# Kernel optimization log

Hardware: AMD Instinct MI355X
Metric: run time of the kernel (lower is better)

Reference implementation:

```python
import jax, jax.numpy as jnp
import numpy as np

N_TOKENS = 65536   # number of embeddings to quantize
CODE_DIM = 768     # embedding dim
NUM_CODES = 4096   # codebook size


def setup_inputs() -> dict:
    key = jax.random.key(0)
    k1, k2 = jax.random.split(key)
    x = jax.random.normal(k1, (N_TOKENS, CODE_DIM), dtype=jnp.float32)
    codebook = jax.random.normal(k2, (NUM_CODES, CODE_DIM), dtype=jnp.float32)
    return {"x": x, "codebook": codebook}


def reference(x, codebook):
    # argmin over squared distances == argmin over cdist (sqrt is monotone).
    x2 = jnp.sum(x * x, axis=-1, keepdims=True)          # [N, 1]
    c2 = jnp.sum(codebook * codebook, axis=-1)           # [K]
    dist = x2 + c2[None, :] - 2.0 * jnp.einsum('nd,kd->nk', x, codebook)  # [N, K]
    indices = jnp.argmin(dist, axis=-1)                  # [N] int
    quantized = codebook[indices]                        # gather [N, D]
    # straight-through estimator: forward = quantized, grad flows to x
    q_ste = x + jax.lax.stop_gradient(quantized - x)
    return q_ste, indices
```

## Files before the change

kernel.cpp:

```cpp
#include <hip/hip_runtime.h>

#define N_TOKENS  65536
#define CODE_DIM  768
#define NUM_CODES 4096

#define MARGIN 0.006f
#define FLTMAX 3.4028235e38f

typedef __attribute__((ext_vector_type(8))) short bf16x8;
typedef __attribute__((ext_vector_type(4))) float f32x4;

__device__ __forceinline__ unsigned short f2bf(float f) {
  unsigned int u = __float_as_uint(f);
  unsigned int r = (u + 0x7fffu + ((u >> 16) & 1u)) >> 16;
  return (unsigned short)r;
}
__device__ __forceinline__ float bf2f(unsigned short h) {
  return __uint_as_float(((unsigned int)h) << 16);
}
__device__ __forceinline__ void gl2lds16(const void* g, void* l) {
  __builtin_amdgcn_global_load_lds(
      (const __attribute__((address_space(1))) unsigned int*)g,
      (__attribute__((address_space(3))) unsigned int*)l, 16, 0, 0);
}

__global__ __launch_bounds__(256) void vq_convert_kernel(
    const float* __restrict__ x, const float* __restrict__ cb,
    unsigned short* __restrict__ xh, unsigned short* __restrict__ xl,
    unsigned short* __restrict__ cbh, unsigned short* __restrict__ cbl,
    float* __restrict__ x2, float* __restrict__ c2, int* __restrict__ fcnt) {
  if (blockIdx.x == 0 && threadIdx.x == 0) *fcnt = 0;
  const int wave = threadIdx.x >> 6;
  const int lane = threadIdx.x & 63;
  const int row  = blockIdx.x * 4 + wave;
  const float* src;
  unsigned short *hdst, *ldst;
  float* ndst;
  if (row < N_TOKENS) {
    src = x + (size_t)row * CODE_DIM;
    hdst = xh + (size_t)row * CODE_DIM;
    ldst = xl + (size_t)row * CODE_DIM;
    ndst = x2 + row;
  } else {
    const int r = row - N_TOKENS;
    if (r >= NUM_CODES) return;
    src = cb + (size_t)r * CODE_DIM;
    hdst = cbh + (size_t)r * CODE_DIM;
    ldst = cbl + (size_t)r * CODE_DIM;
    ndst = c2 + r;
  }
  const float4* s4 = (const float4*)src;
  ushort4* h4 = (ushort4*)hdst;
  ushort4* l4 = (ushort4*)ldst;
  float acc = 0.f;
#pragma unroll
  for (int i = 0; i < 3; ++i) {
    float4 f = s4[lane + 64 * i];
    ushort4 h, l;
    h.x = f2bf(f.x); l.x = f2bf(f.x - bf2f(h.x));
    h.y = f2bf(f.y); l.y = f2bf(f.y - bf2f(h.y));
    h.z = f2bf(f.z); l.z = f2bf(f.z - bf2f(h.z));
    h.w = f2bf(f.w); l.w = f2bf(f.w - bf2f(h.w));
    h4[lane + 64 * i] = h;
    l4[lane + 64 * i] = l;
    acc += (f.x * f.x + f.y * f.y) + (f.z * f.z + f.w * f.w);
  }
#pragma unroll
  for (int off = 32; off > 0; off >>= 1) acc += __shfl_down(acc, off, 64);
  if (lane == 0) *ndst = acc;
}

#define BT 256

__global__ __launch_bounds__(512, 2) void vq_mfma_kernel(
    const unsigned short* __restrict__ xh, const unsigned short* __restrict__ xl,
    const unsigned short* __restrict__ cbh, const unsigned short* __restrict__ cbl,
    const float* __restrict__ c2, int* __restrict__ out_idx,
    int* __restrict__ fcnt, int* __restrict__ flist) {
  __shared__ __align__(16) unsigned short sA[3][BT * 64];
  __shared__ __align__(16) unsigned short sB[3][128 * 64];
  __shared__ float redv[512], redsv[512];
  __shared__ int   redi[512];

  const int tid = threadIdx.x;
  const int wave = tid >> 6, lane = tid & 63;
  const int l15 = lane & 15, quad = lane >> 4;
  const int wr = wave >> 1, wc = wave & 1;
  const int tokBase = blockIdx.x * BT;

  const int lr = lane >> 3;
  const int cc = (lane & 7) ^ lr;
  const int hsel = cc >> 2;
  const int coff = (cc & 3) * 8;
  const unsigned short* pAsrc = hsel ? xl : xh;
  const unsigned short* pBsrc = hsel ? cbl : cbh;
  const size_t aOff = (size_t)(tokBase + wave * 32 + lr) * CODE_DIM + coff;
  const size_t bOff = (size_t)(wave * 16 + lr) * CODE_DIM + coff;

  const int aposh = (quad ^ (l15 & 7)) * 8;
  const int aBaseH = (wr * 64 + l15) * 64 + aposh;
  const int aBaseL = (wr * 64 + l15) * 64 + (aposh ^ 32);
  const int bBaseH = (wc * 64 + l15) * 64 + aposh;
  const int bBaseL = (wc * 64 + l15) * 64 + (aposh ^ 32);

  float v[4][4], sv[4][4];
  int bi[4][4];
#pragma unroll
  for (int i = 0; i < 4; ++i)
#pragma unroll
    for (int r = 0; r < 4; ++r) { v[i][r] = FLTMAX; sv[i][r] = FLTMAX; bi[i][r] = 0; }

  auto STAGE = [&](int slot, int sk0, size_t bbase) {
#pragma unroll
    for (int t = 0; t < 4; ++t)
      gl2lds16(pAsrc + aOff + (size_t)t * (8 * CODE_DIM) + sk0,
               &sA[slot][(wave * 32 + t * 8) * 64]);
#pragma unroll
    for (int t = 0; t < 2; ++t)
      gl2lds16(pBsrc + bbase + bOff + (size_t)t * (8 * CODE_DIM) + sk0,
               &sB[slot][(wave * 16 + t * 8) * 64]);
  };

  STAGE(0, 0, 0);
  STAGE(1, 32, 0);
  asm volatile("s_waitcnt vmcnt(6)" ::: "memory");
  __builtin_amdgcn_s_barrier();
  __builtin_amdgcn_sched_barrier(0);

  int skt = 0, sks = 2;
  for (int kt = 0; kt < NUM_CODES / 128; ++kt) {
    f32x4 acc[4][4];
#pragma unroll
    for (int i = 0; i < 4; ++i)
#pragma unroll
      for (int j = 0; j < 4; ++j) acc[i][j] = (f32x4){0.f, 0.f, 0.f, 0.f};

    for (int ksq = 0; ksq < CODE_DIM / 32; ++ksq) {
      const int slot = ksq % 3;
      const bool more = !(kt == NUM_CODES / 128 - 1 && ksq >= 22);
      if (more) {
        STAGE((ksq + 2) % 3, sks * 32, (size_t)skt * (128 * CODE_DIM));
        if (++sks == CODE_DIM / 32) { sks = 0; ++skt; }
      }

      const unsigned short* As = sA[slot];
      const unsigned short* Bs = sB[slot];
      bf16x8 fah[4], fal[4], fbh[4], fbl[4];
#pragma unroll
      for (int i = 0; i < 4; ++i) {
        fah[i] = *(const bf16x8*)(As + aBaseH + i * 1024);
        fal[i] = *(const bf16x8*)(As + aBaseL + i * 1024);
      }
#pragma unroll
      for (int j = 0; j < 4; ++j) {
        fbh[j] = *(const bf16x8*)(Bs + bBaseH + j * 1024);
        fbl[j] = *(const bf16x8*)(Bs + bBaseL + j * 1024);
      }
      __builtin_amdgcn_s_setprio(1);
#pragma unroll
      for (int i = 0; i < 4; ++i)
#pragma unroll
        for (int j = 0; j < 4; ++j) {
          acc[i][j] = __builtin_amdgcn_mfma_f32_16x16x32_bf16(fah[i], fbh[j], acc[i][j], 0, 0, 0);
          acc[i][j] = __builtin_amdgcn_mfma_f32_16x16x32_bf16(fah[i], fbl[j], acc[i][j], 0, 0, 0);
          acc[i][j] = __builtin_amdgcn_mfma_f32_16x16x32_bf16(fal[i], fbh[j], acc[i][j], 0, 0, 0);
        }
      __builtin_amdgcn_s_setprio(0);
      if (more) asm volatile("s_waitcnt vmcnt(6)" ::: "memory");
      else      asm volatile("s_waitcnt vmcnt(0)" ::: "memory");
      __builtin_amdgcn_s_barrier();
      __builtin_amdgcn_sched_barrier(0);
    }

    const int kbase = kt * 128;
#pragma unroll
    for (int j = 0; j < 4; ++j) {
      const int kcol = kbase + wc * 64 + j * 16 + l15;
      const float c2j = c2[kcol];
#pragma unroll
      for (int i = 0; i < 4; ++i)
#pragma unroll
        for (int r = 0; r < 4; ++r) {
          float s = fmaf(-2.0f, acc[i][j][r], c2j);
          float vo = v[i][r];
          sv[i][r] = fminf(sv[i][r], fmaxf(s, vo));
          bool lt = s < vo;
          v[i][r]  = lt ? s : vo;
          bi[i][r] = lt ? kcol : bi[i][r];
        }
    }
  }

#pragma unroll
  for (int i = 0; i < 4; ++i)
#pragma unroll
    for (int r = 0; r < 4; ++r) {
      float vv = v[i][r], svv = sv[i][r];
      int ii = bi[i][r];
#pragma unroll
      for (int m = 1; m < 16; m <<= 1) {
        float ov = __shfl_xor(vv, m, 64);
        float osv = __shfl_xor(svv, m, 64);
        int oi = __shfl_xor(ii, m, 64);
        float nsv = fminf(fminf(svv, osv), fmaxf(vv, ov));
        bool take = (ov < vv) || (ov == vv && oi < ii);
        vv = take ? ov : vv;
        ii = take ? oi : ii;
        svv = nsv;
      }
      if (l15 == 0) {
        int row = wr * 64 + i * 16 + quad * 4 + r;
        redv[row * 2 + wc] = vv;
        redsv[row * 2 + wc] = svv;
        redi[row * 2 + wc] = ii;
      }
    }
  __syncthreads();
  if (tid < 256) {
    float v0 = redv[tid * 2], v1 = redv[tid * 2 + 1];
    float s0 = redsv[tid * 2], s1 = redsv[tid * 2 + 1];
    int i0 = redi[tid * 2], i1 = redi[tid * 2 + 1];
    bool take = (v1 < v0) || (v1 == v0 && i1 < i0);
    float bv = take ? v1 : v0;
    int bidx = take ? i1 : i0;
    float bsv = fminf(fminf(s0, s1), fmaxf(v0, v1));
    out_idx[tokBase + tid] = bidx;
    if (bsv - bv < MARGIN) {
      int p = atomicAdd(fcnt, 1);
      flist[p] = tokBase + tid;
    }
  }
}

__global__ __launch_bounds__(256) void vq_rescan_kernel(
    const float* __restrict__ x, const float* __restrict__ cb,
    const float* __restrict__ x2, const float* __restrict__ c2,
    const int* __restrict__ fcnt, const int* __restrict__ flist,
    int* __restrict__ out_idx) {
  __shared__ float xs[CODE_DIM];
  __shared__ float rv[256];
  __shared__ int ri[256];
  const int nf = *fcnt;
  for (int f = blockIdx.x; f < nf; f += gridDim.x) {
    const int tok = flist[f];
    __syncthreads();
    if (threadIdx.x < 192)
      ((float4*)xs)[threadIdx.x] = ((const float4*)(x + (size_t)tok * CODE_DIM))[threadIdx.x];
    __syncthreads();
    const float xx = x2[tok];
    float bv = FLTMAX;
    int bidx = 0;
    for (int kk = 0; kk < NUM_CODES / 256; ++kk) {
      const int k = kk * 256 + threadIdx.x;
      const float4* crow = (const float4*)(cb + (size_t)k * CODE_DIM);
      float acc = 0.f;
      for (int c = 0; c < CODE_DIM / 4; ++c) {
        float4 cv = crow[c];
        float4 xv = ((float4*)xs)[c];
        acc += (xv.x * cv.x + xv.y * cv.y) + (xv.z * cv.z + xv.w * cv.w);
      }
      float dist = (xx + c2[k]) - 2.0f * acc;
      if (dist < bv) { bv = dist; bidx = k; }
    }
    rv[threadIdx.x] = bv;
    ri[threadIdx.x] = bidx;
    __syncthreads();
    for (int s = 128; s > 0; s >>= 1) {
      if (threadIdx.x < s) {
        float ov = rv[threadIdx.x + s];
        int oi = ri[threadIdx.x + s];
        if (ov < rv[threadIdx.x] || (ov == rv[threadIdx.x] && oi < ri[threadIdx.x])) {
          rv[threadIdx.x] = ov;
          ri[threadIdx.x] = oi;
        }
      }
      __syncthreads();
    }
    if (threadIdx.x == 0) out_idx[tok] = ri[0];
  }
}

__global__ __launch_bounds__(256) void vq_gather_kernel(
    const float* __restrict__ cb, const int* __restrict__ idx,
    float* __restrict__ out) {
  const int wave = threadIdx.x >> 6;
  const int lane = threadIdx.x & 63;
  const int token = blockIdx.x * 4 + wave;
  const int k = idx[token];
  const float4* src = (const float4*)(cb + (size_t)k * CODE_DIM);
  float4* dst = (float4*)(out + (size_t)token * CODE_DIM);
#pragma unroll
  for (int i = 0; i < 3; ++i) dst[lane + 64 * i] = src[lane + 64 * i];
  if (lane == 0) out[(size_t)N_TOKENS * CODE_DIM + token] = (float)k;
}

#define MT 64
#define KT 128
#define DT 32
#define LDSTRIDE 36

__global__ __launch_bounds__(256) void vq_norms_kernel(
    const float* __restrict__ x, const float* __restrict__ cb,
    float* __restrict__ x2, float* __restrict__ c2) {
  const int wave = threadIdx.x >> 6;
  const int lane = threadIdx.x & 63;
  const int row = blockIdx.x * 4 + wave;
  const float* src;
  float* dst;
  if (row < N_TOKENS) {
    src = x + (size_t)row * CODE_DIM;
    dst = x2 + row;
  } else {
    const int r = row - N_TOKENS;
    if (r >= NUM_CODES) return;
    src = cb + (size_t)r * CODE_DIM;
    dst = c2 + r;
  }
  const float4* s4 = (const float4*)src;
  float acc = 0.f;
#pragma unroll
  for (int i = 0; i < 3; ++i) {
    float4 vv = s4[lane + 64 * i];
    acc += (vv.x * vv.x + vv.y * vv.y) + (vv.z * vv.z + vv.w * vv.w);
  }
#pragma unroll
  for (int off = 32; off > 0; off >>= 1) acc += __shfl_down(acc, off, 64);
  if (lane == 0) *dst = acc;
}

__global__ __launch_bounds__(256) void vq_argmin_kernel(
    const float* __restrict__ x, const float* __restrict__ cb,
    const float* __restrict__ x2, const float* __restrict__ c2,
    int* __restrict__ out_idx) {
  __shared__ float xs[MT * LDSTRIDE];
  __shared__ float cs[KT * LDSTRIDE];
  __shared__ float x2s[MT];
  __shared__ float c2s[KT];
  const int tid = threadIdx.x;
  const int tx = tid & 15;
  const int ty = tid >> 4;
  const int tokBase = blockIdx.x * MT;
  if (tid < MT) x2s[tid] = x2[tokBase + tid];
  float bestv[4];
  int besti[4];
#pragma unroll
  for (int i = 0; i < 4; ++i) { bestv[i] = FLTMAX; besti[i] = 0; }
  const float4* xg = (const float4*)x;
  const float4* cg = (const float4*)cb;
  for (int kt = 0; kt < NUM_CODES / KT; ++kt) {
    const int kBase = kt * KT;
    __syncthreads();
    if (tid < KT) c2s[tid] = c2[kBase + tid];
    float acc[4][8];
#pragma unroll
    for (int i = 0; i < 4; ++i)
#pragma unroll
      for (int j = 0; j < 8; ++j) acc[i][j] = 0.f;
    for (int dc = 0; dc < CODE_DIM / DT; ++dc) {
      __syncthreads();
#pragma unroll
      for (int r = 0; r < 2; ++r) {
        int fidx = tid + 256 * r;
        int row = fidx >> 3, c4 = fidx & 7;
        float4 vv = xg[(size_t)(tokBase + row) * (CODE_DIM / 4) + dc * 8 + c4];
        *(float4*)&xs[row * LDSTRIDE + c4 * 4] = vv;
      }
#pragma unroll
      for (int r = 0; r < 4; ++r) {
        int fidx = tid + 256 * r;
        int row = fidx >> 3, c4 = fidx & 7;
        float4 vv = cg[(size_t)(kBase + row) * (CODE_DIM / 4) + dc * 8 + c4];
        *(float4*)&cs[row * LDSTRIDE + c4 * 4] = vv;
      }
      __syncthreads();
#pragma unroll
      for (int dd = 0; dd < DT / 4; ++dd) {
        float4 xv[4], cv[8];
#pragma unroll
        for (int i = 0; i < 4; ++i)
          xv[i] = *(const float4*)&xs[(ty + 16 * i) * LDSTRIDE + dd * 4];
#pragma unroll
        for (int j = 0; j < 8; ++j)
          cv[j] = *(const float4*)&cs[(tx + 16 * j) * LDSTRIDE + dd * 4];
#pragma unroll
        for (int i = 0; i < 4; ++i)
#pragma unroll
          for (int j = 0; j < 8; ++j)
            acc[i][j] += (xv[i].x * cv[j].x + xv[i].y * cv[j].y) +
                         (xv[i].z * cv[j].z + xv[i].w * cv[j].w);
      }
    }
#pragma unroll
    for (int i = 0; i < 4; ++i) {
      const float xx = x2s[ty + 16 * i];
#pragma unroll
      for (int j = 0; j < 8; ++j) {
        float dist = (xx + c2s[tx + 16 * j]) - 2.0f * acc[i][j];
        int k = kBase + tx + 16 * j;
        if (dist < bestv[i]) { bestv[i] = dist; besti[i] = k; }
      }
    }
  }
  __syncthreads();
  float* rdv = xs;
  int* rdi = (int*)cs;
#pragma unroll
  for (int i = 0; i < 4; ++i) {
    const int m = ty + 16 * i;
    rdv[m * 16 + tx] = bestv[i];
    rdi[m * 16 + tx] = besti[i];
  }
  __syncthreads();
  if (tid < MT) {
    float bv = rdv[tid * 16];
    int bidx = rdi[tid * 16];
#pragma unroll
    for (int t = 1; t < 16; ++t) {
      float vv = rdv[tid * 16 + t];
      int kk = rdi[tid * 16 + t];
      if (vv < bv || (vv == bv && kk < bidx)) { bv = vv; bidx = kk; }
    }
    out_idx[tokBase + tid] = bidx;
  }
}

extern "C" void kernel_launch(void* const* d_in, const int* in_sizes, int n_in,
                              void* d_out, int out_size, void* d_ws, size_t ws_size,
                              hipStream_t stream) {
  (void)in_sizes; (void)n_in; (void)out_size;
  const float* x = (const float*)d_in[0];
  const float* cb = (const float*)d_in[1];
  float* out = (float*)d_out;

  char* w = (char*)d_ws;
  unsigned short* xh = (unsigned short*)w;  w += (size_t)N_TOKENS * CODE_DIM * 2;
  unsigned short* xl = (unsigned short*)w;  w += (size_t)N_TOKENS * CODE_DIM * 2;
  unsigned short* cbh = (unsigned short*)w; w += (size_t)NUM_CODES * CODE_DIM * 2;
  unsigned short* cbl = (unsigned short*)w; w += (size_t)NUM_CODES * CODE_DIM * 2;
  float* x2 = (float*)w;  w += (size_t)N_TOKENS * 4;
  float* c2 = (float*)w;  w += (size_t)NUM_CODES * 4;
  int* idx = (int*)w;     w += (size_t)N_TOKENS * 4;
  int* flist = (int*)w;   w += (size_t)N_TOKENS * 4;
  int* fcnt = (int*)w;    w += 256;
  const size_t need = (size_t)(w - (char*)d_ws);

  if (ws_size >= need) {
    vq_convert_kernel<<<(N_TOKENS + NUM_CODES) / 4, 256, 0, stream>>>(
        x, cb, xh, xl, cbh, cbl, x2, c2, fcnt);
    vq_mfma_kernel<<<N_TOKENS / BT, 512, 0, stream>>>(
        xh, xl, cbh, cbl, c2, idx, fcnt, flist);
    vq_rescan_kernel<<<512, 256, 0, stream>>>(x, cb, x2, c2, fcnt, flist, idx);
    vq_gather_kernel<<<N_TOKENS / 4, 256, 0, stream>>>(cb, idx, out);
  } else {
    float* fx2 = (float*)d_ws;
    float* fc2 = fx2 + N_TOKENS;
    int* fidx = (int*)(fc2 + NUM_CODES);
    vq_norms_kernel<<<(N_TOKENS + NUM_CODES + 3) / 4, 256, 0, stream>>>(x, cb, fx2, fc2);
    vq_argmin_kernel<<<N_TOKENS / MT, 256, 0, stream>>>(x, cb, fx2, fc2, fidx);
    vq_gather_kernel<<<N_TOKENS / 4, 256, 0, stream>>>(cb, fidx, out);
  }
}
```

Measured before the change: 2.100 ms.

## Interleave LDS fragment loads and global prefetch with MFMA quadrants

Splits each k-step's 4x4 MFMA block into four 2x2 quadrants. LDS fragment reads and the global-to-LDS prefetch issues are spread between the quadrants, with extra barriers between phases, so memory traffic overlaps with matrix math in a ping-pong schedule. The staging condition moves to a global step counter. The extra workgroup barriers per step add sync cost and could stall waves if the phases are imbalanced.

```diff
diff --git a/kernel.cpp b/kernel.cpp
--- a/kernel.cpp
+++ b/kernel.cpp
@@ -72,6 +72,22 @@
 
 #define BT 256
 
+template <int IB, int JB>
+__device__ __forceinline__ void mfquad(f32x4 (&acc)[4][4], const bf16x8 (&fah)[4],
+                                       const bf16x8 (&fal)[4], const bf16x8 (&fbh)[4],
+                                       const bf16x8 (&fbl)[4]) {
+  __builtin_amdgcn_s_setprio(1);
+#pragma unroll
+  for (int i = IB; i < IB + 2; ++i)
+#pragma unroll
+    for (int j = JB; j < JB + 2; ++j) {
+      acc[i][j] = __builtin_amdgcn_mfma_f32_16x16x32_bf16(fah[i], fbh[j], acc[i][j], 0, 0, 0);
+      acc[i][j] = __builtin_amdgcn_mfma_f32_16x16x32_bf16(fah[i], fbl[j], acc[i][j], 0, 0, 0);
+      acc[i][j] = __builtin_amdgcn_mfma_f32_16x16x32_bf16(fal[i], fbh[j], acc[i][j], 0, 0, 0);
+    }
+  __builtin_amdgcn_s_setprio(0);
+}
+
 __global__ __launch_bounds__(512, 2) void vq_mfma_kernel(
     const unsigned short* __restrict__ xh, const unsigned short* __restrict__ xl,
     const unsigned short* __restrict__ cbh, const unsigned short* __restrict__ cbl,
@@ -110,7 +126,7 @@
 #pragma unroll
     for (int r = 0; r < 4; ++r) { v[i][r] = FLTMAX; sv[i][r] = FLTMAX; bi[i][r] = 0; }
 
-  auto STAGE = [&](int slot, int sk0, size_t bbase) {
+  auto STAGE6 = [&](int slot, int sk0, size_t bbase) {
 #pragma unroll
     for (int t = 0; t < 4; ++t)
       gl2lds16(pAsrc + aOff + (size_t)t * (8 * CODE_DIM) + sk0,
@@ -121,8 +137,8 @@
                &sB[slot][(wave * 16 + t * 8) * 64]);
   };
 
-  STAGE(0, 0, 0);
-  STAGE(1, 32, 0);
+  STAGE6(0, 0, 0);
+  STAGE6(1, 32, 0);
   asm volatile("s_waitcnt vmcnt(6)" ::: "memory");
   __builtin_amdgcn_s_barrier();
   __builtin_amdgcn_sched_barrier(0);
@@ -137,35 +153,61 @@
 
     for (int ksq = 0; ksq < CODE_DIM / 32; ++ksq) {
       const int slot = ksq % 3;
-      const bool more = !(kt == NUM_CODES / 128 - 1 && ksq >= 22);
-      if (more) {
-        STAGE((ksq + 2) % 3, sks * 32, (size_t)skt * (128 * CODE_DIM));
-        if (++sks == CODE_DIM / 32) { sks = 0; ++skt; }
-      }
-
+      const int gstep = kt * 24 + ksq;
+      const bool more = (gstep <= 765);
       const unsigned short* As = sA[slot];
       const unsigned short* Bs = sB[slot];
+      const int ssl = (ksq + 2) % 3;
+      const int ssk0 = sks * 32;
+      const size_t sbb = (size_t)skt * (128 * (size_t)CODE_DIM);
+
       bf16x8 fah[4], fal[4], fbh[4], fbl[4];
 #pragma unroll
-      for (int i = 0; i < 4; ++i) {
+      for (int i = 0; i < 2; ++i) {
         fah[i] = *(const bf16x8*)(As + aBaseH + i * 1024);
         fal[i] = *(const bf16x8*)(As + aBaseL + i * 1024);
       }
 #pragma unroll
-      for (int j = 0; j < 4; ++j) {
+      for (int j = 0; j < 2; ++j) {
         fbh[j] = *(const bf16x8*)(Bs + bBaseH + j * 1024);
         fbl[j] = *(const bf16x8*)(Bs + bBaseL + j * 1024);
       }
-      __builtin_amdgcn_s_setprio(1);
-#pragma unroll
-      for (int i = 0; i < 4; ++i)
-#pragma unroll
-        for (int j = 0; j < 4; ++j) {
-          acc[i][j] = __builtin_amdgcn_mfma_f32_16x16x32_bf16(fah[i], fbh[j], acc[i][j], 0, 0, 0);
-          acc[i][j] = __builtin_amdgcn_mfma_f32_16x16x32_bf16(fah[i], fbl[j], acc[i][j], 0, 0, 0);
-          acc[i][j] = __builtin_amdgcn_mfma_f32_16x16x32_bf16(fal[i], fbh[j], acc[i][j], 0, 0, 0);
-        }
-      __builtin_amdgcn_s_setprio(0);
+      if (more) {
+        gl2lds16(pAsrc + aOff + (size_t)0 * (8 * CODE_DIM) + ssk0, &sA[ssl][(wave * 32 + 0) * 64]);
+        gl2lds16(pAsrc + aOff + (size_t)1 * (8 * CODE_DIM) + ssk0, &sA[ssl][(wave * 32 + 8) * 64]);
+      }
+      __builtin_amdgcn_s_barrier();
+      mfquad<0, 0>(acc, fah, fal, fbh, fbl);
+      __builtin_amdgcn_s_barrier();
+      __builtin_amdgcn_sched_barrier(0);
+#pragma unroll
+      for (int j = 2; j < 4; ++j) {
+        fbh[j] = *(const bf16x8*)(Bs + bBaseH + j * 1024);
+        fbl[j] = *(const bf16x8*)(Bs + bBaseL + j * 1024);
+      }
+      if (more) {
+        gl2lds16(pAsrc + aOff + (size_t)2 * (8 * CODE_DIM) + ssk0, &sA[ssl][(wave * 32 + 16) * 64]);
+        gl2lds16(pAsrc + aOff + (size_t)3 * (8 * CODE_DIM) + ssk0, &sA[ssl][(wave * 32 + 24) * 64]);
+      }
+      __builtin_amdgcn_s_barrier();
+      mfquad<0, 2>(acc, fah, fal, fbh, fbl);
+      __builtin_amdgcn_s_barrier();
+      __builtin_amdgcn_sched_barrier(0);
+#pragma unroll
+      for (int i = 2; i < 4; ++i) {
+        fah[i] = *(const bf16x8*)(As + aBaseH + i * 1024);
+        fal[i] = *(const bf16x8*)(As + aBaseL + i * 1024);
+      }
+      if (more) {
+        gl2lds16(pBsrc + sbb + bOff + (size_t)0 * (8 * CODE_DIM) + ssk0, &sB[ssl][(wave * 16 + 0) * 64]);
+        gl2lds16(pBsrc + sbb + bOff + (size_t)1 * (8 * CODE_DIM) + ssk0, &sB[ssl][(wave * 16 + 8) * 64]);
+      }
+      __builtin_amdgcn_s_barrier();
+      mfquad<2, 2>(acc, fah, fal, fbh, fbl);
+      __builtin_amdgcn_s_barrier();
+      __builtin_amdgcn_sched_barrier(0);
+      if (more) { if (++sks == CODE_DIM / 32) { sks = 0; ++skt; } }
+      mfquad<2, 0>(acc, fah, fal, fbh, fbl);
       if (more) asm volatile("s_waitcnt vmcnt(6)" ::: "memory");
       else      asm volatile("s_waitcnt vmcnt(0)" ::: "memory");
       __builtin_amdgcn_s_barrier();
```

Measured after the change: 1.994 ms. 1.05x faster.

## Widen codebook tile to 256, double-buffer LDS, batch rescan tokens by four

Applied to the files above, without the earlier changes.

The main MFMA kernel now covers 256 codes per tile instead of 128, so each wave holds a 4x8 accumulator block. This halves how often the A (token) tile is re-read from LDS per code and cuts the number of tile epilogues. The staging pipeline drops from triple to double buffering with a full vmcnt(0) wait each step, which exposes more load latency, and the larger accumulator raises register pressure at 2 blocks per CU. The rescan kernel now handles four flagged tokens per block, so each codebook row it loads is reused four times.

```diff
diff --git a/kernel.cpp b/kernel.cpp
--- a/kernel.cpp
+++ b/kernel.cpp
@@ -71,14 +71,18 @@
 }
 
 #define BT 256
+#define KTILE 256
+#define NKT (NUM_CODES / KTILE)
+#define NSTEP (CODE_DIM / 32)
+#define TOTSTEP (NKT * NSTEP)
 
 __global__ __launch_bounds__(512, 2) void vq_mfma_kernel(
     const unsigned short* __restrict__ xh, const unsigned short* __restrict__ xl,
     const unsigned short* __restrict__ cbh, const unsigned short* __restrict__ cbl,
     const float* __restrict__ c2, int* __restrict__ out_idx,
     int* __restrict__ fcnt, int* __restrict__ flist) {
-  __shared__ __align__(16) unsigned short sA[3][BT * 64];
-  __shared__ __align__(16) unsigned short sB[3][128 * 64];
+  __shared__ __align__(16) unsigned short sA[2][BT * 64];
+  __shared__ __align__(16) unsigned short sB[2][KTILE * 64];
   __shared__ float redv[512], redsv[512];
   __shared__ int   redi[512];
 
@@ -95,13 +99,13 @@
   const unsigned short* pAsrc = hsel ? xl : xh;
   const unsigned short* pBsrc = hsel ? cbl : cbh;
   const size_t aOff = (size_t)(tokBase + wave * 32 + lr) * CODE_DIM + coff;
-  const size_t bOff = (size_t)(wave * 16 + lr) * CODE_DIM + coff;
+  const size_t bOff = (size_t)(wave * 32 + lr) * CODE_DIM + coff;
 
   const int aposh = (quad ^ (l15 & 7)) * 8;
   const int aBaseH = (wr * 64 + l15) * 64 + aposh;
   const int aBaseL = (wr * 64 + l15) * 64 + (aposh ^ 32);
-  const int bBaseH = (wc * 64 + l15) * 64 + aposh;
-  const int bBaseL = (wc * 64 + l15) * 64 + (aposh ^ 32);
+  const int bBaseH = (wc * 128 + l15) * 64 + aposh;
+  const int bBaseL = (wc * 128 + l15) * 64 + (aposh ^ 32);
 
   float v[4][4], sv[4][4];
   int bi[4][4];
@@ -110,72 +114,75 @@
 #pragma unroll
     for (int r = 0; r < 4; ++r) { v[i][r] = FLTMAX; sv[i][r] = FLTMAX; bi[i][r] = 0; }
 
-  auto STAGE = [&](int slot, int sk0, size_t bbase) {
+  auto STAGE = [&](int slot, int s) {
+    const int sk0 = (s % NSTEP) * 32;
+    const size_t sbb = (size_t)(s / NSTEP) * (KTILE * (size_t)CODE_DIM);
 #pragma unroll
     for (int t = 0; t < 4; ++t)
       gl2lds16(pAsrc + aOff + (size_t)t * (8 * CODE_DIM) + sk0,
                &sA[slot][(wave * 32 + t * 8) * 64]);
 #pragma unroll
-    for (int t = 0; t < 2; ++t)
-      gl2lds16(pBsrc + bbase + bOff + (size_t)t * (8 * CODE_DIM) + sk0,
-               &sB[slot][(wave * 16 + t * 8) * 64]);
+    for (int t = 0; t < 4; ++t)
+      gl2lds16(pBsrc + sbb + bOff + (size_t)t * (8 * CODE_DIM) + sk0,
+               &sB[slot][(wave * 32 + t * 8) * 64]);
   };
 
-  STAGE(0, 0, 0);
-  STAGE(1, 32, 0);
-  asm volatile("s_waitcnt vmcnt(6)" ::: "memory");
+  STAGE(0, 0);
+  asm volatile("s_waitcnt vmcnt(0)" ::: "memory");
   __builtin_amdgcn_s_barrier();
   __builtin_amdgcn_sched_barrier(0);
 
-  int skt = 0, sks = 2;
-  for (int kt = 0; kt < NUM_CODES / 128; ++kt) {
-    f32x4 acc[4][4];
+  for (int kt = 0; kt < NKT; ++kt) {
+    f32x4 acc[4][8];
 #pragma unroll
     for (int i = 0; i < 4; ++i)
 #pragma unroll
-      for (int j = 0; j < 4; ++j) acc[i][j] = (f32x4){0.f, 0.f, 0.f, 0.f};
-
-    for (int ksq = 0; ksq < CODE_DIM / 32; ++ksq) {
-      const int slot = ksq % 3;
-      const bool more = !(kt == NUM_CODES / 128 - 1 && ksq >= 22);
-      if (more) {
-        STAGE((ksq + 2) % 3, sks * 32, (size_t)skt * (128 * CODE_DIM));
-        if (++sks == CODE_DIM / 32) { sks = 0; ++skt; }
-      }
-
-      const unsigned short* As = sA[slot];
-      const unsigned short* Bs = sB[slot];
-      bf16x8 fah[4], fal[4], fbh[4], fbl[4];
+      for (int j = 0; j < 8; ++j) acc[i][j] = (f32x4){0.f, 0.f, 0.f, 0.f};
+
+    for (int ksq = 0; ksq < NSTEP; ++ksq) {
+      const int gstep = kt * NSTEP + ksq;
+      const int cur = gstep & 1;
+      const bool more = (gstep < TOTSTEP - 1);
+      if (more) STAGE(cur ^ 1, gstep + 1);
+
+      const unsigned short* As = sA[cur];
+      const unsigned short* Bs = sB[cur];
+      bf16x8 fah[4], fal[4];
 #pragma unroll
       for (int i = 0; i < 4; ++i) {
         fah[i] = *(const bf16x8*)(As + aBaseH + i * 1024);
         fal[i] = *(const bf16x8*)(As + aBaseL + i * 1024);
       }
 #pragma unroll
-      for (int j = 0; j < 4; ++j) {
-        fbh[j] = *(const bf16x8*)(Bs + bBaseH + j * 1024);
-        fbl[j] = *(const bf16x8*)(Bs + bBaseL + j * 1024);
-      }
-      __builtin_amdgcn_s_setprio(1);
-#pragma unroll
-      for (int i = 0; i < 4; ++i)
-#pragma unroll
-        for (int j = 0; j < 4; ++j) {
-          acc[i][j] = __builtin_amdgcn_mfma_f32_16x16x32_bf16(fah[i], fbh[j], acc[i][j], 0, 0, 0);
-          acc[i][j] = __builtin_amdgcn_mfma_f32_16x16x32_bf16(fah[i], fbl[j], acc[i][j], 0, 0, 0);
-          acc[i][j] = __builtin_amdgcn_mfma_f32_16x16x32_bf16(fal[i], fbh[j], acc[i][j], 0, 0, 0);
+      for (int jp = 0; jp < 4; ++jp) {
+        bf16x8 fbh[2], fbl[2];
+#pragma unroll
+        for (int jj = 0; jj < 2; ++jj) {
+          const int j = jp * 2 + jj;
+          fbh[jj] = *(const bf16x8*)(Bs + bBaseH + j * 1024);
+          fbl[jj] = *(const bf16x8*)(Bs + bBaseL + j * 1024);
         }
-      __builtin_amdgcn_s_setprio(0);
-      if (more) asm volatile("s_waitcnt vmcnt(6)" ::: "memory");
-      else      asm volatile("s_waitcnt vmcnt(0)" ::: "memory");
+        __builtin_amdgcn_s_setprio(1);
+#pragma unroll
+        for (int i = 0; i < 4; ++i)
+#pragma unroll
+          for (int jj = 0; jj < 2; ++jj) {
+            const int j = jp * 2 + jj;
+            acc[i][j] = __builtin_amdgcn_mfma_f32_16x16x32_bf16(fah[i], fbh[jj], acc[i][j], 0, 0, 0);
+            acc[i][j] = __builtin_amdgcn_mfma_f32_16x16x32_bf16(fah[i], fbl[jj], acc[i][j], 0, 0, 0);
+            acc[i][j] = __builtin_amdgcn_mfma_f32_16x16x32_bf16(fal[i], fbh[jj], acc[i][j], 0, 0, 0);
+          }
+        __builtin_amdgcn_s_setprio(0);
+      }
+      asm volatile("s_waitcnt vmcnt(0)" ::: "memory");
       __builtin_amdgcn_s_barrier();
       __builtin_amdgcn_sched_barrier(0);
     }
 
-    const int kbase = kt * 128;
-#pragma unroll
-    for (int j = 0; j < 4; ++j) {
-      const int kcol = kbase + wc * 64 + j * 16 + l15;
+    const int kbase = kt * KTILE;
+#pragma unroll
+    for (int j = 0; j < 8; ++j) {
+      const int kcol = kbase + wc * 128 + j * 16 + l15;
       const float c2j = c2[kcol];
 #pragma unroll
       for (int i = 0; i < 4; ++i)
@@ -237,46 +244,72 @@
     const float* __restrict__ x2, const float* __restrict__ c2,
     const int* __restrict__ fcnt, const int* __restrict__ flist,
     int* __restrict__ out_idx) {
-  __shared__ float xs[CODE_DIM];
+  __shared__ float xs[4][CODE_DIM];
   __shared__ float rv[256];
   __shared__ int ri[256];
   const int nf = *fcnt;
-  for (int f = blockIdx.x; f < nf; f += gridDim.x) {
-    const int tok = flist[f];
+  const int ngr = (nf + 3) >> 2;
+  for (int g = blockIdx.x; g < ngr; g += gridDim.x) {
+    const int base = g * 4;
+    int tok[4];
+#pragma unroll
+    for (int t = 0; t < 4; ++t) tok[t] = flist[min(base + t, nf - 1)];
     __syncthreads();
-    if (threadIdx.x < 192)
-      ((float4*)xs)[threadIdx.x] = ((const float4*)(x + (size_t)tok * CODE_DIM))[threadIdx.x];
+    if (threadIdx.x < 192) {
+#pragma unroll
+      for (int t = 0; t < 4; ++t)
+        ((float4*)xs[t])[threadIdx.x] =
+            ((const float4*)(x + (size_t)tok[t] * CODE_DIM))[threadIdx.x];
+    }
     __syncthreads();
-    const float xx = x2[tok];
-    float bv = FLTMAX;
-    int bidx = 0;
+    float bv[4]; int bidx[4];
+#pragma unroll
+    for (int t = 0; t < 4; ++t) { bv[t] = FLTMAX; bidx[t] = 0; }
     for (int kk = 0; kk < NUM_CODES / 256; ++kk) {
       const int k = kk * 256 + threadIdx.x;
       const float4* crow = (const float4*)(cb + (size_t)k * CODE_DIM);
-      float acc = 0.f;
+      float a0 = 0.f, a1 = 0.f, a2 = 0.f, a3 = 0.f;
       for (int c = 0; c < CODE_DIM / 4; ++c) {
         float4 cv = crow[c];
-        float4 xv = ((float4*)xs)[c];
-        acc += (xv.x * cv.x + xv.y * cv.y) + (xv.z * cv.z + xv.w * cv.w);
-      }
-      float dist = (xx + c2[k]) - 2.0f * acc;
-      if (dist < bv) { bv = dist; bidx = k; }
-    }
-    rv[threadIdx.x] = bv;
-    ri[threadIdx.x] = bidx;
-    __syncthreads();
-    for (int s = 128; s > 0; s >>= 1) {
-      if (threadIdx.x < s) {
-        float ov = rv[threadIdx.x + s];
-        int oi = ri[threadIdx.x + s];
-        if (ov < rv[threadIdx.x] || (ov == rv[threadIdx.x] && oi < ri[threadIdx.x])) {
-          rv[threadIdx.x] = ov;
-          ri[threadIdx.x] = oi;
+        float4 x0 = ((float4*)xs[0])[c];
+        float4 x1 = ((float4*)xs[1])[c];
+        float4 x2v = ((float4*)xs[2])[c];
+        float4 x3 = ((float4*)xs[3])[c];
+        a0 += (x0.x * cv.x + x0.y * cv.y) + (x0.z * cv.z + x0.w * cv.w);
+        a1 += (x1.x * cv.x + x1.y * cv.y) + (x1.z * cv.z + x1.w * cv.w);
+        a2 += (x2v.x * cv.x + x2v.y * cv.y) + (x2v.z * cv.z + x2v.w * cv.w);
+        a3 += (x3.x * cv.x + x3.y * cv.y) + (x3.z * cv.z + x3.w * cv.w);
+      }
+      const float c2k = c2[k];
+      float d0 = (x2[tok[0]] + c2k) - 2.0f * a0;
+      float d1 = (x2[tok[1]] + c2k) - 2.0f * a1;
+      float d2 = (x2[tok[2]] + c2k) - 2.0f * a2;
+      float d3 = (x2[tok[3]] + c2k) - 2.0f * a3;
+      if (d0 < bv[0]) { bv[0] = d0; bidx[0] = k; }
+      if (d1 < bv[1]) { bv[1] = d1; bidx[1] = k; }
+      if (d2 < bv[2]) { bv[2] = d2; bidx[2] = k; }
+      if (d3 < bv[3]) { bv[3] = d3; bidx[3] = k; }
+    }
+#pragma unroll
+    for (int t = 0; t < 4; ++t) {
+      __syncthreads();
+      rv[threadIdx.x] = bv[t];
+      ri[threadIdx.x] = bidx[t];
+      __syncthreads();
+      for (int s = 128; s > 0; s >>= 1) {
+        if (threadIdx.x < s) {
+          float ov = rv[threadIdx.x + s];
+          int oi = ri[threadIdx.x + s];
+          if (ov < rv[threadIdx.x] ||
+              (ov == rv[threadIdx.x] && oi < ri[threadIdx.x])) {
+            rv[threadIdx.x] = ov;
+            ri[threadIdx.x] = oi;
+          }
         }
-      }
-      __syncthreads();
-    }
-    if (threadIdx.x == 0) out_idx[tok] = ri[0];
+        __syncthreads();
+      }
+      if (threadIdx.x == 0 && base + t < nf) out_idx[tok[t]] = ri[0];
+    }
   }
 }
 
```

After: 1.818 ms. 1.15x faster.
